# Optimization experiments

Measured on AMD Instinct MI355X. Metric: run time of the kernel, lower is better.

## Reference

```python
import jax, jax.numpy as jnp
import numpy as np

MAX_AREA_WIDTH = 3  # from init_kwargs


def _window_vals(val, width, merge):
    """Multi-scale forward window sums: for each w in 1..width, sum val[t:t+w]
    over the seq axis, concatenated along the seq axis (total length
    width*L - width*(width-1)/2). Equivalent to the torch recurrence."""
    B, H, L, D = val.shape
    csum = jnp.concatenate(
        [jnp.zeros((B, H, 1, D), val.dtype), jnp.cumsum(val, axis=2)], axis=2)
    parts = []
    for i in range(width):
        w = i + 1
        s = csum[:, :, w:, :] - csum[:, :, :L - w + 1, :]  # [B,H,L-i,D]
        if merge == 'mean':
            s = s / jnp.asarray(w, val.dtype)
        parts.append(s)
    return jnp.concatenate(parts, axis=2)


def _window_masks(mask, width, zero_pad):
    parts = [mask[:, :, :, i:] for i in range(width)]
    m = jnp.concatenate(parts, axis=-1)  # [B,H,L,L']
    if zero_pad:
        m = m.at[:, :, 0, :].set(0)
    return m


def setup_inputs() -> dict:
    key = jax.random.key(0)
    kq, kk, kv = jax.random.split(key, 3)
    B, H, L, D = 8, 8, 512, 64
    q = jax.random.normal(kq, (B, H, L, D), jnp.float32)
    k = jax.random.normal(kk, (B, H, L, D), jnp.float32)
    v = jax.random.normal(kv, (B, H, L, D), jnp.float32)
    # causal attention mask, as used in pykt knowledge-tracing models
    mask = jnp.broadcast_to(jnp.tril(jnp.ones((L, L), jnp.int32)), (B, H, L, L))
    return {"q": q, "k": k, "v": v, "d_k": 64, "mask": mask, "zero_pad": 1}


def reference(q, k, v, d_k, mask, zero_pad):
    W = MAX_AREA_WIDTH
    k_area = _window_vals(k, W, 'mean')   # [B,H,L',D]
    v_area = _window_vals(v, W, 'sum')    # [B,H,L',D]
    m = _window_masks(mask, W, zero_pad)  # [B,H,L,L']
    scores = jnp.einsum('bhqd,bhkd->bhqk', q, k_area) / jnp.sqrt(
        jnp.asarray(d_k, jnp.float32))
    scores = jnp.where(m == 0, jnp.asarray(-1e32, scores.dtype), scores)
    attn = jax.nn.softmax(scores, axis=-1)  # dropout omitted (eval / p=0)
    return jnp.einsum('bhqk,bhkd->bhqd', attn, v_area)
```

## Files before the change

### kernel.cpp

```cpp
#include <hip/hip_runtime.h>


#define LSEQ 512
#define DDIM 64
#define SPB 88
#define SSW 68
#define PSTRIDE 528

typedef __attribute__((ext_vector_type(8))) short bf8_t;
typedef __attribute__((ext_vector_type(4))) float f32x4;

__device__ __forceinline__ unsigned short f2bf(float f) {
  union { float f; unsigned u; } v; v.f = f;
  unsigned u = v.u;
  unsigned r = u + 0x7fffu + ((u >> 16) & 1u);
  return (unsigned short)(r >> 16);
}
__device__ __forceinline__ float bf2f(unsigned short h) {
  union { unsigned u; float f; } v; v.u = ((unsigned)h) << 16; return v.f;
}
__device__ __forceinline__ unsigned pk2(float a, float b) {
  return (unsigned)f2bf(a) | ((unsigned)f2bf(b) << 16);
}
__device__ __forceinline__ float ex2(float x) {
  float r; asm("v_exp_f32 %0, %1" : "=v"(r) : "v"(x)); return r;
}

__global__ __launch_bounds__(256)
void prep_kernel(const float* __restrict__ qg, const float* __restrict__ kg,
                 const float* __restrict__ vg,
                 unsigned short* __restrict__ vt,
                 unsigned short* __restrict__ qbf,
                 unsigned short* __restrict__ kbf,
                 float* __restrict__ outg) {
  const int bid = blockIdx.x, tid = threadIdx.x;
  if (bid < 512) {
    __shared__ float Ts[64][65];
    const int bh = bid >> 3, oct = bid & 7;
    const int t0 = oct * 64;
    const float* vb = vg + (size_t)bh * LSEQ * DDIM;
    unsigned short* vo = vt + (size_t)bh * DDIM * LSEQ;
#pragma unroll
    for (int it = 0; it < 4; ++it) {
      int f = tid + it * 256;
      int t = f >> 4, d4 = f & 15;
      float4 x = ((const float4*)(vb + (size_t)(t0 + t) * DDIM))[d4];
      Ts[d4 * 4 + 0][t] = x.x;
      Ts[d4 * 4 + 1][t] = x.y;
      Ts[d4 * 4 + 2][t] = x.z;
      Ts[d4 * 4 + 3][t] = x.w;
    }
    __syncthreads();
    const int d = tid >> 2, tg = tid & 3;
    unsigned pk[8];
#pragma unroll
    for (int j = 0; j < 8; ++j)
      pk[j] = pk2(Ts[d][tg * 16 + 2 * j], Ts[d][tg * 16 + 2 * j + 1]);
    uint4* dst = (uint4*)&vo[(size_t)d * LSEQ + t0 + tg * 16];
    dst[0] = make_uint4(pk[0], pk[1], pk[2], pk[3]);
    dst[1] = make_uint4(pk[4], pk[5], pk[6], pk[7]);
  } else if (bid < 1536) {
    const bool isq = bid < 1024;
    const float4* src = (const float4*)(isq ? qg : kg);
    ushort4* dst = (ushort4*)(isq ? qbf : kbf);
    const float s = isq ? 0.125f : 1.0f;
    const int blk = bid & 511;
#pragma unroll
    for (int it = 0; it < 4; ++it) {
      int f = blk * 1024 + it * 256 + tid;
      float4 x = src[f];
      ushort4 o;
      o.x = f2bf(x.x * s); o.y = f2bf(x.y * s);
      o.z = f2bf(x.z * s); o.w = f2bf(x.w * s);
      dst[f] = o;
    }
  } else {
    __shared__ float4 red[256];
    const int bh = bid - 1536;
    const float4* vb4 = (const float4*)(vg + (size_t)bh * LSEQ * DDIM);
    const int d4 = tid & 15, rg = tid >> 4;
    float4 acc = make_float4(0.f, 0.f, 0.f, 0.f);
    for (int t = rg; t < LSEQ; t += 16) {
      float c = (t == 0 || t == LSEQ - 1) ? 3.f
              : (t == 1 || t == LSEQ - 2) ? 5.f : 6.f;
      float4 x = vb4[t * 16 + d4];
      acc.x += c * x.x; acc.y += c * x.y; acc.z += c * x.z; acc.w += c * x.w;
    }
    red[rg * 16 + d4] = acc;
    __syncthreads();
    if (rg == 0) {
      float4 sum = make_float4(0.f, 0.f, 0.f, 0.f);
#pragma unroll
      for (int g = 0; g < 16; ++g) {
        float4 x = red[g * 16 + d4];
        sum.x += x.x; sum.y += x.y; sum.z += x.z; sum.w += x.w;
      }
      const float inv = 1.0f / 1533.0f;
      sum.x *= inv; sum.y *= inv; sum.z *= inv; sum.w *= inv;
      ((float4*)(outg + (size_t)bh * LSEQ * DDIM))[d4] = sum;
    }
  }
}

__global__ __launch_bounds__(256, 4)
void area_task_kernel(const unsigned short* __restrict__ qbf,
                      const unsigned short* __restrict__ kbf,
                      const unsigned short* __restrict__ vtg,
                      float* __restrict__ partials) {
  __shared__ __align__(16) float Ss[4][16][SSW];
  __shared__ __align__(16) unsigned short Ps[4][16 * SPB];

  const int w = threadIdx.x >> 6, lane = threadIdx.x & 63;
  const int tau = blockIdx.x * 4 + w;
  const int bh = tau / 144;
  const int idx = tau - bh * 144;
  int g = 0;
  while (2 * (g + 1) * (g + 2) <= idx) ++g;
  const int rem = idx - 2 * g * (g + 1);
  const int dq = rem / (g + 1);
  const int qt = 4 * g + dq;
  const int kt = rem - dq * (g + 1);
  const int q0 = qt * 16, t0 = kt * 64;

  const int lc = lane & 15, lg = lane >> 4;
  const int koff = lg * 8;
  const int pr = lane >> 2, ps = lane & 3;
  const int ec0 = ps * 16;
  const float L2E = 1.44269504088896341f;

  const unsigned short* qb = qbf + (size_t)bh * LSEQ * DDIM;
  const unsigned short* kb = kbf + (size_t)bh * LSEQ * DDIM;
  const unsigned short* vtb = vtg + (size_t)bh * DDIM * LSEQ;

  const bf8_t qa0 = *(const bf8_t*)&qb[(size_t)(q0 + lc) * DDIM + koff];
  const bf8_t qa1 = *(const bf8_t*)&qb[(size_t)(q0 + lc) * DDIM + 32 + koff];

  float val = 0.f;
  if (kt > 0) {
    const int prr = lane >> 2, jj = (lane >> 1) & 1, hh = lane & 1;
    const unsigned short* qrow = qb + (size_t)(q0 + prr) * DDIM + 32 * hh;
    const unsigned short* krow = kb + (size_t)(t0 - 2 + jj) * DDIM + 32 * hh;
#pragma unroll
    for (int b4 = 0; b4 < 4; ++b4) {
      bf8_t qv = *(const bf8_t*)&qrow[b4 * 8];
      bf8_t kv = *(const bf8_t*)&krow[b4 * 8];
#pragma unroll
      for (int e = 0; e < 8; ++e)
        val = fmaf(bf2f((unsigned short)qv[e]), bf2f((unsigned short)kv[e]), val);
    }
    val += __shfl_xor(val, 1);
  }
  const float ctx2 = __shfl(val, lane & ~3);
  const float ctx1 = __shfl(val, (lane & ~3) | 2);

#pragma unroll
  for (int nt = 0; nt < 4; ++nt) {
    const size_t kr = (size_t)(t0 + nt * 16 + lc) * DDIM;
    bf8_t kf0 = *(const bf8_t*)&kb[kr + koff];
    bf8_t kf1 = *(const bf8_t*)&kb[kr + 32 + koff];
    f32x4 acc = (f32x4){0.f, 0.f, 0.f, 0.f};
    acc = __builtin_amdgcn_mfma_f32_16x16x32_bf16(qa0, kf0, acc, 0, 0, 0);
    acc = __builtin_amdgcn_mfma_f32_16x16x32_bf16(qa1, kf1, acc, 0, 0, 0);
#pragma unroll
    for (int r = 0; r < 4; ++r)
      Ss[w][4 * lg + r][nt * 16 + lc] = acc[r];
  }

  float lrow;
  {
    const int vmax = q0 + pr - t0;
    float pm1, pm2;
    if (ps == 0) {
      pm1 = (kt ? ctx1 : -1.0e30f) * L2E;
      pm2 = (kt ? ctx2 : -1.0e30f) * L2E;
    } else {
      pm1 = Ss[w][pr][ec0 - 1] * L2E;
      pm2 = Ss[w][pr][ec0 - 2] * L2E;
    }

    float sv[16];
    *(float4*)&sv[0]  = *(const float4*)&Ss[w][pr][ec0];
    *(float4*)&sv[4]  = *(const float4*)&Ss[w][pr][ec0 + 4];
    *(float4*)&sv[8]  = *(const float4*)&Ss[w][pr][ec0 + 8];
    *(float4*)&sv[12] = *(const float4*)&Ss[w][pr][ec0 + 12];
#pragma unroll
    for (int k = 0; k < 16; ++k) sv[k] *= L2E;

    float cf[18];
#pragma unroll
    for (int k = 0; k < 18; ++k) cf[k] = 0.f;
    float ladd = 0.f;
    {
      float a1 = pm1, a2 = pm2;
#pragma unroll
      for (int k = 0; k < 16; ++k) {
        float s0 = sv[k];
        bool vld = (ec0 + k) <= vmax;
        float t = a1 + s0;
        float p1 = vld ? ex2(s0) : 0.f;
        float p2 = vld ? ex2(0.5f * t) : 0.f;
        float p3 = vld ? ex2((1.0f / 3.0f) * (a2 + t)) : 0.f;
        float p23 = p2 + p3, p123 = p1 + p23;
        ladd += p123;
        cf[k + 2] += p123;
        cf[k + 1] += p23;
        cf[k]     += p3;
        a2 = a1; a1 = s0;
      }
    }
    ladd += __shfl_xor(ladd, 1);
    ladd += __shfl_xor(ladd, 2);
    lrow = ladd;

    float up16 = __shfl_up(cf[16], 1, 4);
    float up17 = __shfl_up(cf[17], 1, 4);
    if (ps > 0) { cf[0] += up16; cf[1] += up17; }

    const int base = pr * SPB;
    if (ps == 0) {
      *(unsigned*)&Ps[w][base + 64] = pk2(cf[0], cf[1]);
#pragma unroll
      for (int j = 0; j < 7; ++j)
        *(unsigned*)&Ps[w][base + 2 * j] = pk2(cf[2 + 2 * j], cf[3 + 2 * j]);
    } else {
      const int tcb = 16 * ps - 2;
#pragma unroll
      for (int j = 0; j < 8; ++j)
        *(unsigned*)&Ps[w][base + tcb + 2 * j] = pk2(cf[2 * j], cf[2 * j + 1]);
      if (ps == 3) *(unsigned*)&Ps[w][base + 62] = pk2(cf[16], cf[17]);
    }
  }

  f32x4 oacc[4];
#pragma unroll
  for (int nt = 0; nt < 4; ++nt) oacc[nt] = (f32x4){0.f, 0.f, 0.f, 0.f};
  {
    bf8_t pa0 = *(const bf8_t*)&Ps[w][lc * SPB + koff];
    bf8_t pa1 = *(const bf8_t*)&Ps[w][lc * SPB + 32 + koff];
    float cm2[4], cm1[4];
#pragma unroll
    for (int r = 0; r < 4; ++r) {
      unsigned pc = *(const unsigned*)&Ps[w][(4 * lg + r) * SPB + 64];
      cm2[r] = bf2f((unsigned short)(pc & 0xffffu));
      cm1[r] = bf2f((unsigned short)(pc >> 16));
    }
#pragma unroll
    for (int nt = 0; nt < 4; ++nt) {
      const size_t vr = (size_t)(nt * 16 + lc) * LSEQ + t0;
      bf8_t vf0 = *(const bf8_t*)&vtb[vr + koff];
      bf8_t vf1 = *(const bf8_t*)&vtb[vr + 32 + koff];
      oacc[nt] = __builtin_amdgcn_mfma_f32_16x16x32_bf16(pa0, vf0, oacc[nt], 0, 0, 0);
      oacc[nt] = __builtin_amdgcn_mfma_f32_16x16x32_bf16(pa1, vf1, oacc[nt], 0, 0, 0);
      unsigned vc = 0;
      if (kt > 0) vc = *(const unsigned*)&vtb[vr - 2];
      float vm2 = bf2f((unsigned short)(vc & 0xffffu));
      float vm1 = bf2f((unsigned short)(vc >> 16));
#pragma unroll
      for (int r = 0; r < 4; ++r)
        oacc[nt][r] += cm2[r] * vm2 + cm1[r] * vm1;
    }
  }

  {
    float* pb = partials + (size_t)tau * PSTRIDE;
    unsigned pk[8];
#pragma unroll
    for (int nt = 0; nt < 4; ++nt) {
      pk[2 * nt]     = pk2(oacc[nt][0], oacc[nt][1]);
      pk[2 * nt + 1] = pk2(oacc[nt][2], oacc[nt][3]);
    }
    uint4* ob = (uint4*)((unsigned short*)pb + lane * 16);
    ob[0] = make_uint4(pk[0], pk[1], pk[2], pk[3]);
    ob[1] = make_uint4(pk[4], pk[5], pk[6], pk[7]);
    if (ps == 0) pb[512 + pr] = lrow;
  }
}

__global__ __launch_bounds__(256)
void area_reduce_kernel(const float* __restrict__ partials,
                        float* __restrict__ outg) {
  const int w = threadIdx.x >> 6, lane = threadIdx.x & 63;
  const int pair = blockIdx.x * 4 + w;
  const int bh = pair >> 5, qt = pair & 31;
  const int g = qt >> 2, n = g + 1;
  const int start = bh * 144 + 2 * g * (g + 1) + (qt - 4 * g) * (g + 1);
  const int lc = lane & 15, lg = lane >> 4;

  float acc[16];
#pragma unroll
  for (int e = 0; e < 16; ++e) acc[e] = 0.f;
  float la[4] = {0.f, 0.f, 0.f, 0.f};
  for (int t = 0; t < n; ++t) {
    const float* pp = partials + (size_t)(start + t) * PSTRIDE;
    const uint4* ob = (const uint4*)((const unsigned short*)pp + lane * 16);
    uint4 a = ob[0], b = ob[1];
    const unsigned pkv[8] = {a.x, a.y, a.z, a.w, b.x, b.y, b.z, b.w};
#pragma unroll
    for (int j = 0; j < 8; ++j) {
      acc[2 * j]     += bf2f((unsigned short)(pkv[j] & 0xffffu));
      acc[2 * j + 1] += bf2f((unsigned short)(pkv[j] >> 16));
    }
#pragma unroll
    for (int r = 0; r < 4; ++r) la[r] += pp[512 + 4 * lg + r];
  }
#pragma unroll
  for (int r = 0; r < 4; ++r) {
    int gr = qt * 16 + 4 * lg + r;
    if (gr != 0) {
      float inv = 1.0f / la[r];
#pragma unroll
      for (int nt = 0; nt < 4; ++nt)
        outg[((size_t)bh * LSEQ + gr) * DDIM + nt * 16 + lc] = acc[nt * 4 + r] * inv;
    }
  }
}

extern "C" void kernel_launch(void* const* d_in, const int* in_sizes, int n_in,
                              void* d_out, int out_size, void* d_ws, size_t ws_size,
                              hipStream_t stream) {
  (void)in_sizes; (void)n_in; (void)ws_size; (void)out_size;
  const float* q = (const float*)d_in[0];
  const float* k = (const float*)d_in[1];
  const float* v = (const float*)d_in[2];
  float* out = (float*)d_out;

  unsigned short* ws = (unsigned short*)d_ws;
  unsigned short* vt  = ws;
  unsigned short* qbf = ws + 2097152;
  unsigned short* kbf = ws + 2 * 2097152;
  float* partials = (float*)(ws + 3 * 2097152);

  prep_kernel<<<dim3(1600), dim3(256), 0, stream>>>(q, k, v, vt, qbf, kbf, out);
  area_task_kernel<<<dim3(2304), dim3(256), 0, stream>>>(qbf, kbf, vt, partials);
  area_reduce_kernel<<<dim3(512), dim3(256), 0, stream>>>(partials, out);
}
```

Baseline: 158.3 us.

## Fuse per-tile attention and cross-tile reduction into one kernel per query tile

Replaces the task-per-warp kernel, with its global bf16 partials and separate reduce kernel, by one block per (bh, q-tile). The four warps stride over key tiles and combine their outputs through shared memory. Q is now converted to bf16 inside the fused kernel instead of in prep. The two boundary scores that were a scalar dot-product context are now taken from an extra MFMA over the previous 16 keys. This removes a launch, the partials round trip and one prep pass, but leaves warps unevenly loaded: later q-tiles have up to 8 key tiles spread over only 4 warps, while early tiles leave warps idle.

Measured after the change: 161.6 us. 1.02x slower.

```diff
diff --git a/kernel.cpp b/kernel.cpp
--- a/kernel.cpp
+++ b/kernel.cpp
@@ -5,7 +5,6 @@
 #define DDIM 64
 #define SPB 88
 #define SSW 68
-#define PSTRIDE 528
 
 typedef __attribute__((ext_vector_type(8))) short bf8_t;
 typedef __attribute__((ext_vector_type(4))) float f32x4;
@@ -25,12 +24,18 @@
 __device__ __forceinline__ float ex2(float x) {
   float r; asm("v_exp_f32 %0, %1" : "=v"(r) : "v"(x)); return r;
 }
+__device__ __forceinline__ bf8_t pack8(float4 a, float4 b, float s) {
+  bf8_t r;
+  r[0] = (short)f2bf(a.x * s); r[1] = (short)f2bf(a.y * s);
+  r[2] = (short)f2bf(a.z * s); r[3] = (short)f2bf(a.w * s);
+  r[4] = (short)f2bf(b.x * s); r[5] = (short)f2bf(b.y * s);
+  r[6] = (short)f2bf(b.z * s); r[7] = (short)f2bf(b.w * s);
+  return r;
+}
 
 __global__ __launch_bounds__(256)
-void prep_kernel(const float* __restrict__ qg, const float* __restrict__ kg,
-                 const float* __restrict__ vg,
+void prep_kernel(const float* __restrict__ kg, const float* __restrict__ vg,
                  unsigned short* __restrict__ vt,
-                 unsigned short* __restrict__ qbf,
                  unsigned short* __restrict__ kbf,
                  float* __restrict__ outg) {
   const int bid = blockIdx.x, tid = threadIdx.x;
@@ -59,24 +64,22 @@
     uint4* dst = (uint4*)&vo[(size_t)d * LSEQ + t0 + tg * 16];
     dst[0] = make_uint4(pk[0], pk[1], pk[2], pk[3]);
     dst[1] = make_uint4(pk[4], pk[5], pk[6], pk[7]);
-  } else if (bid < 1536) {
-    const bool isq = bid < 1024;
-    const float4* src = (const float4*)(isq ? qg : kg);
-    ushort4* dst = (ushort4*)(isq ? qbf : kbf);
-    const float s = isq ? 0.125f : 1.0f;
+  } else if (bid < 1024) {
+    const float4* src = (const float4*)kg;
+    ushort4* dst = (ushort4*)kbf;
     const int blk = bid & 511;
 #pragma unroll
     for (int it = 0; it < 4; ++it) {
       int f = blk * 1024 + it * 256 + tid;
       float4 x = src[f];
       ushort4 o;
-      o.x = f2bf(x.x * s); o.y = f2bf(x.y * s);
-      o.z = f2bf(x.z * s); o.w = f2bf(x.w * s);
+      o.x = f2bf(x.x); o.y = f2bf(x.y);
+      o.z = f2bf(x.z); o.w = f2bf(x.w);
       dst[f] = o;
     }
   } else {
     __shared__ float4 red[256];
-    const int bh = bid - 1536;
+    const int bh = bid - 1024;
     const float4* vb4 = (const float4*)(vg + (size_t)bh * LSEQ * DDIM);
     const int d4 = tid & 15, rg = tid >> 4;
     float4 acc = make_float4(0.f, 0.f, 0.f, 0.f);
@@ -103,214 +106,185 @@
 }
 
 __global__ __launch_bounds__(256, 4)
-void area_task_kernel(const unsigned short* __restrict__ qbf,
-                      const unsigned short* __restrict__ kbf,
-                      const unsigned short* __restrict__ vtg,
-                      float* __restrict__ partials) {
+void area_fused_kernel(const float* __restrict__ qg,
+                       const unsigned short* __restrict__ kbf,
+                       const unsigned short* __restrict__ vtg,
+                       float* __restrict__ outg) {
   __shared__ __align__(16) float Ss[4][16][SSW];
   __shared__ __align__(16) unsigned short Ps[4][16 * SPB];
-
+  __shared__ float Lred[4][16];
+
+  const int bid = blockIdx.x;
+  const int bh = bid >> 5, qt = bid & 31;
+  const int q0 = qt * 16;
   const int w = threadIdx.x >> 6, lane = threadIdx.x & 63;
-  const int tau = blockIdx.x * 4 + w;
-  const int bh = tau / 144;
-  const int idx = tau - bh * 144;
-  int g = 0;
-  while (2 * (g + 1) * (g + 2) <= idx) ++g;
-  const int rem = idx - 2 * g * (g + 1);
-  const int dq = rem / (g + 1);
-  const int qt = 4 * g + dq;
-  const int kt = rem - dq * (g + 1);
-  const int q0 = qt * 16, t0 = kt * 64;
-
   const int lc = lane & 15, lg = lane >> 4;
   const int koff = lg * 8;
   const int pr = lane >> 2, ps = lane & 3;
   const int ec0 = ps * 16;
   const float L2E = 1.44269504088896341f;
 
-  const unsigned short* qb = qbf + (size_t)bh * LSEQ * DDIM;
+  const float* qb = qg + (size_t)bh * LSEQ * DDIM;
   const unsigned short* kb = kbf + (size_t)bh * LSEQ * DDIM;
   const unsigned short* vtb = vtg + (size_t)bh * DDIM * LSEQ;
 
-  const bf8_t qa0 = *(const bf8_t*)&qb[(size_t)(q0 + lc) * DDIM + koff];
-  const bf8_t qa1 = *(const bf8_t*)&qb[(size_t)(q0 + lc) * DDIM + 32 + koff];
-
-  float val = 0.f;
-  if (kt > 0) {
-    const int prr = lane >> 2, jj = (lane >> 1) & 1, hh = lane & 1;
-    const unsigned short* qrow = qb + (size_t)(q0 + prr) * DDIM + 32 * hh;
-    const unsigned short* krow = kb + (size_t)(t0 - 2 + jj) * DDIM + 32 * hh;
-#pragma unroll
-    for (int b4 = 0; b4 < 4; ++b4) {
-      bf8_t qv = *(const bf8_t*)&qrow[b4 * 8];
-      bf8_t kv = *(const bf8_t*)&krow[b4 * 8];
-#pragma unroll
-      for (int e = 0; e < 8; ++e)
-        val = fmaf(bf2f((unsigned short)qv[e]), bf2f((unsigned short)kv[e]), val);
-    }
-    val += __shfl_xor(val, 1);
+  bf8_t qa0, qa1;
+  {
+    const float* qrp = qb + (size_t)(q0 + lc) * DDIM;
+    qa0 = pack8(*(const float4*)(qrp + koff), *(const float4*)(qrp + koff + 4),
+                0.125f);
+    qa1 = pack8(*(const float4*)(qrp + 32 + koff),
+                *(const float4*)(qrp + 36 + koff), 0.125f);
   }
-  const float ctx2 = __shfl(val, lane & ~3);
-  const float ctx1 = __shfl(val, (lane & ~3) | 2);
-
-#pragma unroll
-  for (int nt = 0; nt < 4; ++nt) {
-    const size_t kr = (size_t)(t0 + nt * 16 + lc) * DDIM;
-    bf8_t kf0 = *(const bf8_t*)&kb[kr + koff];
-    bf8_t kf1 = *(const bf8_t*)&kb[kr + 32 + koff];
-    f32x4 acc = (f32x4){0.f, 0.f, 0.f, 0.f};
-    acc = __builtin_amdgcn_mfma_f32_16x16x32_bf16(qa0, kf0, acc, 0, 0, 0);
-    acc = __builtin_amdgcn_mfma_f32_16x16x32_bf16(qa1, kf1, acc, 0, 0, 0);
+
+  f32x4 oacc[4];
+#pragma unroll
+  for (int nt = 0; nt < 4; ++nt) oacc[nt] = (f32x4){0.f, 0.f, 0.f, 0.f};
+  float ltot = 0.f;
+
+  const int n = (qt >> 2) + 1;
+  for (int kt = w; kt < n; kt += 4) {
+    const int t0 = kt * 64;
+
+    if (kt == 0) {
+      if (ps == 0) { Ss[w][pr][64] = -1.0e30f; Ss[w][pr][65] = -1.0e30f; }
+    } else {
+      const size_t kr = (size_t)(t0 - 16 + lc) * DDIM;
+      bf8_t kp0 = *(const bf8_t*)&kb[kr + koff];
+      bf8_t kp1 = *(const bf8_t*)&kb[kr + 32 + koff];
+      f32x4 a2v = (f32x4){0.f, 0.f, 0.f, 0.f};
+      a2v = __builtin_amdgcn_mfma_f32_16x16x32_bf16(qa0, kp0, a2v, 0, 0, 0);
+      a2v = __builtin_amdgcn_mfma_f32_16x16x32_bf16(qa1, kp1, a2v, 0, 0, 0);
+      if (lc == 14) {
+#pragma unroll
+        for (int r = 0; r < 4; ++r) Ss[w][4 * lg + r][64] = a2v[r];
+      }
+      if (lc == 15) {
+#pragma unroll
+        for (int r = 0; r < 4; ++r) Ss[w][4 * lg + r][65] = a2v[r];
+      }
+    }
+
+#pragma unroll
+    for (int nt = 0; nt < 4; ++nt) {
+      const size_t kr = (size_t)(t0 + nt * 16 + lc) * DDIM;
+      bf8_t kf0 = *(const bf8_t*)&kb[kr + koff];
+      bf8_t kf1 = *(const bf8_t*)&kb[kr + 32 + koff];
+      f32x4 acc = (f32x4){0.f, 0.f, 0.f, 0.f};
+      acc = __builtin_amdgcn_mfma_f32_16x16x32_bf16(qa0, kf0, acc, 0, 0, 0);
+      acc = __builtin_amdgcn_mfma_f32_16x16x32_bf16(qa1, kf1, acc, 0, 0, 0);
+#pragma unroll
+      for (int r = 0; r < 4; ++r)
+        Ss[w][4 * lg + r][nt * 16 + lc] = acc[r];
+    }
+
+    {
+      const int vmax = q0 + pr - t0;
+      float pm1 = Ss[w][pr][ps == 0 ? 65 : ec0 - 1] * L2E;
+      float pm2 = Ss[w][pr][ps == 0 ? 64 : ec0 - 2] * L2E;
+
+      float sv[16];
+      *(float4*)&sv[0]  = *(const float4*)&Ss[w][pr][ec0];
+      *(float4*)&sv[4]  = *(const float4*)&Ss[w][pr][ec0 + 4];
+      *(float4*)&sv[8]  = *(const float4*)&Ss[w][pr][ec0 + 8];
+      *(float4*)&sv[12] = *(const float4*)&Ss[w][pr][ec0 + 12];
+#pragma unroll
+      for (int k = 0; k < 16; ++k) sv[k] *= L2E;
+
+      float cf[18];
+#pragma unroll
+      for (int k = 0; k < 18; ++k) cf[k] = 0.f;
+      float ladd = 0.f;
+      {
+        float a1 = pm1, a2 = pm2;
+#pragma unroll
+        for (int k = 0; k < 16; ++k) {
+          float s0 = sv[k];
+          bool vld = (ec0 + k) <= vmax;
+          float t = a1 + s0;
+          float p1 = vld ? ex2(s0) : 0.f;
+          float p2 = vld ? ex2(0.5f * t) : 0.f;
+          float p3 = vld ? ex2((1.0f / 3.0f) * (a2 + t)) : 0.f;
+          float p23 = p2 + p3, p123 = p1 + p23;
+          ladd += p123;
+          cf[k + 2] += p123;
+          cf[k + 1] += p23;
+          cf[k]     += p3;
+          a2 = a1; a1 = s0;
+        }
+      }
+      ladd += __shfl_xor(ladd, 1);
+      ladd += __shfl_xor(ladd, 2);
+      ltot += ladd;
+
+      float up16 = __shfl_up(cf[16], 1, 4);
+      float up17 = __shfl_up(cf[17], 1, 4);
+      if (ps > 0) { cf[0] += up16; cf[1] += up17; }
+
+      const int base = pr * SPB;
+      if (ps == 0) {
+        *(unsigned*)&Ps[w][base + 64] = pk2(cf[0], cf[1]);
+#pragma unroll
+        for (int j = 0; j < 7; ++j)
+          *(unsigned*)&Ps[w][base + 2 * j] = pk2(cf[2 + 2 * j], cf[3 + 2 * j]);
+      } else {
+        const int tcb = 16 * ps - 2;
+#pragma unroll
+        for (int j = 0; j < 8; ++j)
+          *(unsigned*)&Ps[w][base + tcb + 2 * j] = pk2(cf[2 * j], cf[2 * j + 1]);
+        if (ps == 3) *(unsigned*)&Ps[w][base + 62] = pk2(cf[16], cf[17]);
+      }
+    }
+
+    {
+      bf8_t pa0 = *(const bf8_t*)&Ps[w][lc * SPB + koff];
+      bf8_t pa1 = *(const bf8_t*)&Ps[w][lc * SPB + 32 + koff];
+      float cm2[4], cm1[4];
+#pragma unroll
+      for (int r = 0; r < 4; ++r) {
+        unsigned pc = *(const unsigned*)&Ps[w][(4 * lg + r) * SPB + 64];
+        cm2[r] = bf2f((unsigned short)(pc & 0xffffu));
+        cm1[r] = bf2f((unsigned short)(pc >> 16));
+      }
+#pragma unroll
+      for (int nt = 0; nt < 4; ++nt) {
+        const size_t vr = (size_t)(nt * 16 + lc) * LSEQ + t0;
+        bf8_t vf0 = *(const bf8_t*)&vtb[vr + koff];
+        bf8_t vf1 = *(const bf8_t*)&vtb[vr + 32 + koff];
+        oacc[nt] = __builtin_amdgcn_mfma_f32_16x16x32_bf16(pa0, vf0, oacc[nt], 0, 0, 0);
+        oacc[nt] = __builtin_amdgcn_mfma_f32_16x16x32_bf16(pa1, vf1, oacc[nt], 0, 0, 0);
+        unsigned vc = 0;
+        if (kt > 0) vc = *(const unsigned*)&vtb[vr - 2];
+        float vm2 = bf2f((unsigned short)(vc & 0xffffu));
+        float vm1 = bf2f((unsigned short)(vc >> 16));
+#pragma unroll
+        for (int r = 0; r < 4; ++r)
+          oacc[nt][r] += cm2[r] * vm2 + cm1[r] * vm1;
+      }
+    }
+  }
+
+#pragma unroll
+  for (int nt = 0; nt < 4; ++nt)
 #pragma unroll
     for (int r = 0; r < 4; ++r)
-      Ss[w][4 * lg + r][nt * 16 + lc] = acc[r];
-  }
-
-  float lrow;
+      Ss[w][4 * lg + r][nt * 16 + lc] = oacc[nt][r];
+  if (ps == 0) Lred[w][pr] = ltot;
+  __syncthreads();
+
   {
-    const int vmax = q0 + pr - t0;
-    float pm1, pm2;
-    if (ps == 0) {
-      pm1 = (kt ? ctx1 : -1.0e30f) * L2E;
-      pm2 = (kt ? ctx2 : -1.0e30f) * L2E;
-    } else {
-      pm1 = Ss[w][pr][ec0 - 1] * L2E;
-      pm2 = Ss[w][pr][ec0 - 2] * L2E;
-    }
-
-    float sv[16];
-    *(float4*)&sv[0]  = *(const float4*)&Ss[w][pr][ec0];
-    *(float4*)&sv[4]  = *(const float4*)&Ss[w][pr][ec0 + 4];
-    *(float4*)&sv[8]  = *(const float4*)&Ss[w][pr][ec0 + 8];
-    *(float4*)&sv[12] = *(const float4*)&Ss[w][pr][ec0 + 12];
-#pragma unroll
-    for (int k = 0; k < 16; ++k) sv[k] *= L2E;
-
-    float cf[18];
-#pragma unroll
-    for (int k = 0; k < 18; ++k) cf[k] = 0.f;
-    float ladd = 0.f;
-    {
-      float a1 = pm1, a2 = pm2;
-#pragma unroll
-      for (int k = 0; k < 16; ++k) {
-        float s0 = sv[k];
-        bool vld = (ec0 + k) <= vmax;
-        float t = a1 + s0;
-        float p1 = vld ? ex2(s0) : 0.f;
-        float p2 = vld ? ex2(0.5f * t) : 0.f;
-        float p3 = vld ? ex2((1.0f / 3.0f) * (a2 + t)) : 0.f;
-        float p23 = p2 + p3, p123 = p1 + p23;
-        ladd += p123;
-        cf[k + 2] += p123;
-        cf[k + 1] += p23;
-        cf[k]     += p3;
-        a2 = a1; a1 = s0;
-      }
-    }
-    ladd += __shfl_xor(ladd, 1);
-    ladd += __shfl_xor(ladd, 2);
-    lrow = ladd;
-
-    float up16 = __shfl_up(cf[16], 1, 4);
-    float up17 = __shfl_up(cf[17], 1, 4);
-    if (ps > 0) { cf[0] += up16; cf[1] += up17; }
-
-    const int base = pr * SPB;
-    if (ps == 0) {
-      *(unsigned*)&Ps[w][base + 64] = pk2(cf[0], cf[1]);
-#pragma unroll
-      for (int j = 0; j < 7; ++j)
-        *(unsigned*)&Ps[w][base + 2 * j] = pk2(cf[2 + 2 * j], cf[3 + 2 * j]);
-    } else {
-      const int tcb = 16 * ps - 2;
-#pragma unroll
-      for (int j = 0; j < 8; ++j)
-        *(unsigned*)&Ps[w][base + tcb + 2 * j] = pk2(cf[2 * j], cf[2 * j + 1]);
-      if (ps == 3) *(unsigned*)&Ps[w][base + 62] = pk2(cf[16], cf[17]);
-    }
-  }
-
-  f32x4 oacc[4];
-#pragma unroll
-  for (int nt = 0; nt < 4; ++nt) oacc[nt] = (f32x4){0.f, 0.f, 0.f, 0.f};
-  {
-    bf8_t pa0 = *(const bf8_t*)&Ps[w][lc * SPB + koff];
-    bf8_t pa1 = *(const bf8_t*)&Ps[w][lc * SPB + 32 + koff];
-    float cm2[4], cm1[4];
-#pragma unroll
-    for (int r = 0; r < 4; ++r) {
-      unsigned pc = *(const unsigned*)&Ps[w][(4 * lg + r) * SPB + 64];
-      cm2[r] = bf2f((unsigned short)(pc & 0xffffu));
-      cm1[r] = bf2f((unsigned short)(pc >> 16));
-    }
-#pragma unroll
-    for (int nt = 0; nt < 4; ++nt) {
-      const size_t vr = (size_t)(nt * 16 + lc) * LSEQ + t0;
-      bf8_t vf0 = *(const bf8_t*)&vtb[vr + koff];
-      bf8_t vf1 = *(const bf8_t*)&vtb[vr + 32 + koff];
-      oacc[nt] = __builtin_amdgcn_mfma_f32_16x16x32_bf16(pa0, vf0, oacc[nt], 0, 0, 0);
-      oacc[nt] = __builtin_amdgcn_mfma_f32_16x16x32_bf16(pa1, vf1, oacc[nt], 0, 0, 0);
-      unsigned vc = 0;
-      if (kt > 0) vc = *(const unsigned*)&vtb[vr - 2];
-      float vm2 = bf2f((unsigned short)(vc & 0xffffu));
-      float vm1 = bf2f((unsigned short)(vc >> 16));
-#pragma unroll
-      for (int r = 0; r < 4; ++r)
-        oacc[nt][r] += cm2[r] * vm2 + cm1[r] * vm1;
-    }
-  }
-
-  {
-    float* pb = partials + (size_t)tau * PSTRIDE;
-    unsigned pk[8];
-#pragma unroll
-    for (int nt = 0; nt < 4; ++nt) {
-      pk[2 * nt]     = pk2(oacc[nt][0], oacc[nt][1]);
-      pk[2 * nt + 1] = pk2(oacc[nt][2], oacc[nt][3]);
-    }
-    uint4* ob = (uint4*)((unsigned short*)pb + lane * 16);
-    ob[0] = make_uint4(pk[0], pk[1], pk[2], pk[3]);
-    ob[1] = make_uint4(pk[4], pk[5], pk[6], pk[7]);
-    if (ps == 0) pb[512 + pr] = lrow;
-  }
-}
-
-__global__ __launch_bounds__(256)
-void area_reduce_kernel(const float* __restrict__ partials,
-                        float* __restrict__ outg) {
-  const int w = threadIdx.x >> 6, lane = threadIdx.x & 63;
-  const int pair = blockIdx.x * 4 + w;
-  const int bh = pair >> 5, qt = pair & 31;
-  const int g = qt >> 2, n = g + 1;
-  const int start = bh * 144 + 2 * g * (g + 1) + (qt - 4 * g) * (g + 1);
-  const int lc = lane & 15, lg = lane >> 4;
-
-  float acc[16];
-#pragma unroll
-  for (int e = 0; e < 16; ++e) acc[e] = 0.f;
-  float la[4] = {0.f, 0.f, 0.f, 0.f};
-  for (int t = 0; t < n; ++t) {
-    const float* pp = partials + (size_t)(start + t) * PSTRIDE;
-    const uint4* ob = (const uint4*)((const unsigned short*)pp + lane * 16);
-    uint4 a = ob[0], b = ob[1];
-    const unsigned pkv[8] = {a.x, a.y, a.z, a.w, b.x, b.y, b.z, b.w};
-#pragma unroll
-    for (int j = 0; j < 8; ++j) {
-      acc[2 * j]     += bf2f((unsigned short)(pkv[j] & 0xffffu));
-      acc[2 * j + 1] += bf2f((unsigned short)(pkv[j] >> 16));
-    }
-#pragma unroll
-    for (int r = 0; r < 4; ++r) la[r] += pp[512 + 4 * lg + r];
-  }
-#pragma unroll
-  for (int r = 0; r < 4; ++r) {
-    int gr = qt * 16 + 4 * lg + r;
+    const int row = threadIdx.x >> 4, c4 = threadIdx.x & 15;
+    f32x4 s = (f32x4){0.f, 0.f, 0.f, 0.f};
+    float lsum = 0.f;
+#pragma unroll
+    for (int w2 = 0; w2 < 4; ++w2) {
+      s += *(const f32x4*)&Ss[w2][row][c4 * 4];
+      lsum += Lred[w2][row];
+    }
+    const int gr = q0 + row;
     if (gr != 0) {
-      float inv = 1.0f / la[r];
-#pragma unroll
-      for (int nt = 0; nt < 4; ++nt)
-        outg[((size_t)bh * LSEQ + gr) * DDIM + nt * 16 + lc] = acc[nt * 4 + r] * inv;
+      s *= (1.0f / lsum);
+      *(f32x4*)&outg[((size_t)bh * LSEQ + gr) * DDIM + c4 * 4] = s;
     }
   }
 }
@@ -326,11 +300,8 @@
 
   unsigned short* ws = (unsigned short*)d_ws;
   unsigned short* vt  = ws;
-  unsigned short* qbf = ws + 2097152;
-  unsigned short* kbf = ws + 2 * 2097152;
-  float* partials = (float*)(ws + 3 * 2097152);
-
-  prep_kernel<<<dim3(1600), dim3(256), 0, stream>>>(q, k, v, vt, qbf, kbf, out);
-  area_task_kernel<<<dim3(2304), dim3(256), 0, stream>>>(qbf, kbf, vt, partials);
-  area_reduce_kernel<<<dim3(512), dim3(256), 0, stream>>>(partials, out);
-}
+  unsigned short* kbf = ws + 2097152;
+
+  prep_kernel<<<dim3(1088), dim3(256), 0, stream>>>(k, v, vt, kbf, out);
+  area_fused_kernel<<<dim3(2048), dim3(256), 0, stream>>>(q, kbf, vt, out);
+}
```
